# Performance work log

Measured on AMD Instinct MI355X. Metric: run time of the kernel, lower is better.

## Reference

```python
import jax, jax.numpy as jnp
import numpy as np


def setup_inputs() -> dict:
    key = jax.random.key(0)
    k1, k2, k3, k4 = jax.random.split(key, 4)
    B, S, IN, OUT = 4, 512, 4096, 11008
    x = jax.random.normal(k1, (B, S, IN), dtype=jnp.float32)
    # int8-valued weights stored as int32 (symmetric per-output-channel quant)
    w_int8 = jax.random.randint(k2, (OUT, IN), -128, 128, dtype=jnp.int32)
    # per-output-channel fp32 scales (positive, like absmax/127)
    scales = jax.random.uniform(k3, (OUT,), dtype=jnp.float32, minval=1e-4, maxval=0.05)
    bias = jax.random.normal(k4, (OUT,), dtype=jnp.float32)
    return {"x": x, "w_int8": w_int8, "scales": scales, "bias": bias}


def reference(x, w_int8, scales, bias):
    # On-the-fly dequant: w[o, i] = int8[o, i] * scale[o], then y = x @ w.T + b
    w = (w_int8.astype(jnp.float32) * scales[:, None]).astype(x.dtype)  # [OUT, IN]
    return jnp.einsum('bsi,oi->bso', x, w) + bias
```

## Files before the change

### kernel.cpp

```cpp
#include <hip/hip_runtime.h>
#include <hip/hip_bf16.h>
#include <stdint.h>


typedef __attribute__((ext_vector_type(8))) short short8;
typedef __attribute__((ext_vector_type(4))) float f32x4;
typedef __attribute__((ext_vector_type(4))) float float4v;
typedef __attribute__((ext_vector_type(4))) int int4v;

#define MM 2048
#define NN 11008
#define KK 4096
#define NT (KK / 64)
#define ROWB ((size_t)KK)

static __device__ __forceinline__ ushort f2bf_rne(float f) {
    uint32_t u = __builtin_bit_cast(uint32_t, f);
    u = (u + 0x7FFFu + ((u >> 16) & 1u)) >> 16;
    return (ushort)u;
}
static __device__ __forceinline__ ushort i2bf_exact(int v) {
    return (ushort)(__builtin_bit_cast(uint32_t, (float)v) >> 16);
}
static __device__ __forceinline__ void gload16(const void* g, void* lds) {
    __builtin_amdgcn_global_load_lds(
        (const __attribute__((address_space(1))) uint32_t*)g,
        (__attribute__((address_space(3))) uint32_t*)lds, 16, 0, 0);
}

#define BAR() do { asm volatile("" ::: "memory"); __builtin_amdgcn_s_barrier(); asm volatile("" ::: "memory"); } while (0)

__global__ __launch_bounds__(256)
void rowmax_x(const float* __restrict__ X, float* __restrict__ Sx, float* __restrict__ SxInv) {
    const int r = blockIdx.x;
    const float4v* xr = (const float4v*)(X + (size_t)r * KK);
    float m = 0.f;
    for (int i = threadIdx.x; i < KK / 4; i += 256) {
        float4v v = xr[i];
        m = fmaxf(m, fmaxf(fmaxf(fabsf(v[0]), fabsf(v[1])),
                           fmaxf(fabsf(v[2]), fabsf(v[3]))));
    }
#pragma unroll
    for (int off = 32; off; off >>= 1) m = fmaxf(m, __shfl_down(m, off));
    __shared__ float wmax[4];
    if ((threadIdx.x & 63) == 0) wmax[threadIdx.x >> 6] = m;
    __syncthreads();
    if (threadIdx.x == 0) {
        float a = fmaxf(fmaxf(wmax[0], wmax[1]), fmaxf(wmax[2], wmax[3]));
        Sx[r]    = a / 127.f;
        SxInv[r] = (a > 0.f) ? 127.f / a : 0.f;
    }
}

__global__ __launch_bounds__(256)
void quant_pack(const float* __restrict__ X, const int* __restrict__ W,
                const float* __restrict__ SxInv,
                char* __restrict__ Xq, char* __restrict__ Wq) {
    const int NX4 = MM * KK / 4;
    const int NW4 = NN * KK / 4;
    const int stride = gridDim.x * blockDim.x;
    for (int i = blockIdx.x * blockDim.x + threadIdx.x; i < NX4 + NW4; i += stride) {
        if (i < NX4) {
            float4v v = ((const float4v*)X)[i];
            const float inv = SxInv[i >> 10];
            uint32_t p = 0;
#pragma unroll
            for (int j = 0; j < 4; ++j) {
                int q = (int)rintf(v[j] * inv);
                p |= ((uint32_t)(q & 255)) << (8 * j);
            }
            ((uint32_t*)Xq)[i] = p;
        } else {
            int j = i - NX4;
            int4v w = ((const int4v*)W)[j];
            uint32_t p = ((uint32_t)(w[0] & 255)) | ((uint32_t)(w[1] & 255) << 8) |
                         ((uint32_t)(w[2] & 255) << 16) | ((uint32_t)(w[3] & 255) << 24);
            ((uint32_t*)Wq)[j] = p;
        }
    }
}

static __device__ __forceinline__ void stageA(const char* g, char* lds, int wid, size_t kb) {
    gload16(g + kb,                      lds        + wid * 1024);
    gload16(g + kb + (size_t)64 * ROWB,  lds + 4096 + wid * 1024);
}
static __device__ __forceinline__ void stageB(const char* g, char* lds, int wid, size_t kb) {
#pragma unroll
    for (int c = 0; c < 4; ++c)
        gload16(g + kb + (size_t)(c * 64) * ROWB, lds + c * 4096 + wid * 1024);
}

__global__ __launch_bounds__(256, 2)
void gemm_i8(const char* __restrict__ A, const char* __restrict__ B,
             const float* __restrict__ Sx, const float* __restrict__ S,
             const float* __restrict__ Bv, float* __restrict__ Y) {
    __shared__ char smem[73728];
    char* bA0 = smem;
    char* bA1 = smem + 8192;
    char* bA2 = smem + 16384;
    char* bB0 = smem + 24576;
    char* bB1 = smem + 40960;
    char* bB2 = smem + 57344;

    const int tid  = threadIdx.x;
    const int lane = tid & 63;
    const int wid  = tid >> 6;
    const int l15  = lane & 15;
    const int q    = lane >> 4;

    const int swz  = (blockIdx.x & 7) * 86 + (blockIdx.x >> 3);
    const int brow = (swz / 43) * 128;
    const int bcol = (swz % 43) * 256;

    const int srow4 = tid >> 2;
    const int sslot = (tid & 3) ^ ((srow4 >> 1) & 3);
    const char* gA = A + (size_t)(brow + srow4) * ROWB + sslot * 16;
    const char* gB = B + (size_t)(bcol + srow4) * ROWB + sslot * 16;

    const int kq  = (q ^ ((l15 >> 1) & 3)) * 16;
    const int rdA = l15 * 64;
    const int rdB = (wid * 64 + l15) * 64;

#define LDA(buf, m) (*(const int4v*)((buf) + rdA + (m) * 1024 + kq))
#define LDB(buf, n) (*(const int4v*)((buf) + rdB + (n) * 1024 + kq))

    int4v acc[8][4] = {};

    stageA(gA, bA0, wid, 0);
    stageB(gB, bB0, wid, 0);
    stageA(gA, bA1, wid, 64);
    stageB(gB, bB1, wid, 64);
    asm volatile("s_waitcnt vmcnt(6)" ::: "memory");
    BAR();

    char* cA = bA0; char* nA = bA1; char* pA = bA2;
    char* cB = bB0; char* nB = bB1; char* pB = bB2;

    for (int t = 0; t < NT; ++t) {
        const size_t kb2 = (size_t)((t + 2 < NT) ? t + 2 : NT - 1) * 64;

        int4v af[8], bf[4];
#pragma unroll
        for (int m = 0; m < 8; ++m) af[m] = LDA(cA, m);
#pragma unroll
        for (int n = 0; n < 4; ++n) bf[n] = LDB(cB, n);

        stageA(gA, pA, wid, kb2);
        stageB(gB, pB, wid, kb2);

        __builtin_amdgcn_s_setprio(1);
#pragma unroll
        for (int m = 0; m < 8; ++m)
#pragma unroll
            for (int n = 0; n < 4; ++n)
                acc[m][n] = __builtin_amdgcn_mfma_i32_16x16x64_i8(af[m], bf[n], acc[m][n], 0, 0, 0);
        __builtin_amdgcn_s_setprio(0);

        asm volatile("s_waitcnt vmcnt(6)" ::: "memory");
        BAR();

        char* tmp;
        tmp = cA; cA = nA; nA = pA; pA = tmp;
        tmp = cB; cB = nB; nB = pB; pB = tmp;
    }

#pragma unroll
    for (int n = 0; n < 4; ++n) {
        const int gc = bcol + wid * 64 + n * 16 + l15;
        const float sj = S[gc];
        const float bj = Bv[gc];
#pragma unroll
        for (int m = 0; m < 8; ++m) {
            const int grow = brow + m * 16 + q * 4;
            float* yp = Y + (size_t)grow * NN + gc;
#pragma unroll
            for (int r = 0; r < 4; ++r)
                yp[(size_t)r * NN] = (float)acc[m][n][r] * (Sx[grow + r] * sj) + bj;
        }
    }
#undef LDA
#undef LDB
}

#define BMF 128
#define BKF 32
#define LDW (BKF + 8)
__global__ __launch_bounds__(256, 2)
void int8lin_fused(const float* __restrict__ X, const int* __restrict__ W,
                   const float* __restrict__ S, const float* __restrict__ Bv,
                   float* __restrict__ Y) {
    __shared__ ushort As[BMF][LDW];
    __shared__ ushort Bs[BMF][LDW];
    const int tid = threadIdx.x, lane = tid & 63, wid = tid >> 6;
    const int wm = wid >> 1, wn = wid & 1, l15 = lane & 15, kh = (lane >> 4) * 8;
    const int bm = blockIdx.x & 15, bn = blockIdx.x >> 4;
    const int brow = bm * BMF, bcol = bn * BMF;
    const int srow = tid >> 1, scol = (tid & 1) * 16;
    const float* xg = X + (size_t)(brow + srow) * KK + scol;
    const int*   wg = W + (size_t)(bcol + srow) * KK + scol;
    f32x4 acc[4][4] = {};
    for (int kt = 0; kt < KK / BKF; ++kt) {
        float4v x0 = *(const float4v*)(xg + 0), x1 = *(const float4v*)(xg + 4);
        float4v x2 = *(const float4v*)(xg + 8), x3 = *(const float4v*)(xg + 12);
        int4v w0 = *(const int4v*)(wg + 0), w1 = *(const int4v*)(wg + 4);
        int4v w2 = *(const int4v*)(wg + 8), w3 = *(const int4v*)(wg + 12);
        xg += BKF; wg += BKF;
        short8 xa = { (short)f2bf_rne(x0[0]), (short)f2bf_rne(x0[1]), (short)f2bf_rne(x0[2]), (short)f2bf_rne(x0[3]),
                      (short)f2bf_rne(x1[0]), (short)f2bf_rne(x1[1]), (short)f2bf_rne(x1[2]), (short)f2bf_rne(x1[3]) };
        short8 xb = { (short)f2bf_rne(x2[0]), (short)f2bf_rne(x2[1]), (short)f2bf_rne(x2[2]), (short)f2bf_rne(x2[3]),
                      (short)f2bf_rne(x3[0]), (short)f2bf_rne(x3[1]), (short)f2bf_rne(x3[2]), (short)f2bf_rne(x3[3]) };
        short8 wa = { (short)i2bf_exact(w0[0]), (short)i2bf_exact(w0[1]), (short)i2bf_exact(w0[2]), (short)i2bf_exact(w0[3]),
                      (short)i2bf_exact(w1[0]), (short)i2bf_exact(w1[1]), (short)i2bf_exact(w1[2]), (short)i2bf_exact(w1[3]) };
        short8 wb = { (short)i2bf_exact(w2[0]), (short)i2bf_exact(w2[1]), (short)i2bf_exact(w2[2]), (short)i2bf_exact(w2[3]),
                      (short)i2bf_exact(w3[0]), (short)i2bf_exact(w3[1]), (short)i2bf_exact(w3[2]), (short)i2bf_exact(w3[3]) };
        __syncthreads();
        *(short8*)&As[srow][scol] = xa; *(short8*)&As[srow][scol + 8] = xb;
        *(short8*)&Bs[srow][scol] = wa; *(short8*)&Bs[srow][scol + 8] = wb;
        __syncthreads();
        short8 af2[4], bf4[4];
#pragma unroll
        for (int i = 0; i < 4; ++i) af2[i] = *(const short8*)&As[wm * 64 + i * 16 + l15][kh];
#pragma unroll
        for (int j = 0; j < 4; ++j) bf4[j] = *(const short8*)&Bs[wn * 64 + j * 16 + l15][kh];
#pragma unroll
        for (int i = 0; i < 4; ++i)
#pragma unroll
            for (int j = 0; j < 4; ++j)
                acc[i][j] = __builtin_amdgcn_mfma_f32_16x16x32_bf16(af2[i], bf4[j], acc[i][j], 0, 0, 0);
    }
#pragma unroll
    for (int j = 0; j < 4; ++j) {
        const int gc = bcol + wn * 64 + j * 16 + l15;
        const float sj = S[gc], bj = Bv[gc];
#pragma unroll
        for (int i = 0; i < 4; ++i) {
            const int grow = brow + wm * 64 + i * 16 + (lane >> 4) * 4;
            float* yp = Y + (size_t)grow * NN + gc;
#pragma unroll
            for (int r = 0; r < 4; ++r)
                yp[(size_t)r * NN] = acc[i][j][r] * sj + bj;
        }
    }
}

extern "C" void kernel_launch(void* const* d_in, const int* in_sizes, int n_in,
                              void* d_out, int out_size, void* d_ws, size_t ws_size,
                              hipStream_t stream) {
    const float* x = (const float*)d_in[0];
    const int*   w = (const int*)d_in[1];
    const float* s = (const float*)d_in[2];
    const float* b = (const float*)d_in[3];
    float* y = (float*)d_out;

    const size_t wq_b = (size_t)NN * KK;
    const size_t xq_b = (size_t)MM * KK;
    const size_t need = wq_b + xq_b + 2 * MM * sizeof(float) + 256;
    if (ws_size >= need) {
        char*  Wq    = (char*)d_ws;
        char*  Xq    = Wq + wq_b;
        float* Sx    = (float*)(Xq + xq_b);
        float* SxInv = Sx + MM;
        hipLaunchKernelGGL(rowmax_x,   dim3(MM),   dim3(256), 0, stream, x, Sx, SxInv);
        hipLaunchKernelGGL(quant_pack, dim3(4096), dim3(256), 0, stream, x, w, SxInv, Xq, Wq);
        hipLaunchKernelGGL(gemm_i8, dim3((MM / 128) * (NN / 256)), dim3(256), 0, stream,
                           Xq, Wq, Sx, s, b, y);
    } else {
        hipLaunchKernelGGL(int8lin_fused, dim3((MM / BMF) * (NN / BMF)), dim3(256), 0, stream,
                           x, w, s, b, y);
    }
}
```

Baseline: 178.7 us.

## Software-pipeline LDS fragment loads across K-iterations with double-buffered registers

```diff
diff --git a/kernel.cpp b/kernel.cpp
--- a/kernel.cpp
+++ b/kernel.cpp
@@ -95,12 +95,6 @@
              const float* __restrict__ Sx, const float* __restrict__ S,
              const float* __restrict__ Bv, float* __restrict__ Y) {
     __shared__ char smem[73728];
-    char* bA0 = smem;
-    char* bA1 = smem + 8192;
-    char* bA2 = smem + 16384;
-    char* bB0 = smem + 24576;
-    char* bB1 = smem + 40960;
-    char* bB2 = smem + 57344;
 
     const int tid  = threadIdx.x;
     const int lane = tid & 63;
@@ -125,44 +119,60 @@
 #define LDB(buf, n) (*(const int4v*)((buf) + rdB + (n) * 1024 + kq))
 
     int4v acc[8][4] = {};
-
-    stageA(gA, bA0, wid, 0);
-    stageB(gB, bB0, wid, 0);
-    stageA(gA, bA1, wid, 64);
-    stageB(gB, bB1, wid, 64);
+    int4v afA_a[4], afA_b[4], bf_a[4], bf_b[4], afB[4];
+
+    char* cA = smem;              char* cB = smem + 24576;
+    char* nA = smem + 8192;       char* nB = smem + 40960;
+    char* pA = smem + 16384;      char* pB = smem + 57344;
+
+    stageA(gA, cA, wid, 0);
+    stageB(gB, cB, wid, 0);
+    stageA(gA, nA, wid, 64);
+    stageB(gB, nB, wid, 64);
     asm volatile("s_waitcnt vmcnt(6)" ::: "memory");
     BAR();
-
-    char* cA = bA0; char* nA = bA1; char* pA = bA2;
-    char* cB = bB0; char* nB = bB1; char* pB = bB2;
-
-    for (int t = 0; t < NT; ++t) {
-        const size_t kb2 = (size_t)((t + 2 < NT) ? t + 2 : NT - 1) * 64;
-
-        int4v af[8], bf[4];
-#pragma unroll
-        for (int m = 0; m < 8; ++m) af[m] = LDA(cA, m);
-#pragma unroll
-        for (int n = 0; n < 4; ++n) bf[n] = LDB(cB, n);
-
-        stageA(gA, pA, wid, kb2);
-        stageB(gB, pB, wid, kb2);
-
-        __builtin_amdgcn_s_setprio(1);
-#pragma unroll
-        for (int m = 0; m < 8; ++m)
-#pragma unroll
-            for (int n = 0; n < 4; ++n)
-                acc[m][n] = __builtin_amdgcn_mfma_i32_16x16x64_i8(af[m], bf[n], acc[m][n], 0, 0, 0);
-        __builtin_amdgcn_s_setprio(0);
-
-        asm volatile("s_waitcnt vmcnt(6)" ::: "memory");
-        BAR();
-
-        char* tmp;
-        tmp = cA; cA = nA; nA = pA; pA = tmp;
-        tmp = cB; cB = nB; nB = pB; pB = tmp;
-    }
+#pragma unroll
+    for (int m = 0; m < 4; ++m) afA_a[m] = LDA(cA, m);
+#pragma unroll
+    for (int n = 0; n < 4; ++n) bf_a[n]  = LDB(cB, n);
+
+#define GEMM_ITER(AFAc, BFc, AFAn, BFn, T)                                        \
+    {                                                                             \
+        const int tt = (T);                                                       \
+        const size_t kb2 = (size_t)((tt + 2 < NT) ? tt + 2 : NT - 1) * 64;        \
+        _Pragma("unroll")                                                         \
+        for (int m = 0; m < 4; ++m) afB[m] = LDA(cA, m + 4);                      \
+        __builtin_amdgcn_s_setprio(1);                                            \
+        _Pragma("unroll")                                                         \
+        for (int m = 0; m < 4; ++m)                                               \
+            _Pragma("unroll")                                                     \
+            for (int n = 0; n < 4; ++n)                                           \
+                acc[m][n] = __builtin_amdgcn_mfma_i32_16x16x64_i8(AFAc[m], BFc[n], acc[m][n], 0, 0, 0); \
+        __builtin_amdgcn_s_setprio(0);                                            \
+        stageA(gA, pA, wid, kb2);                                                 \
+        stageB(gB, pB, wid, kb2);                                                 \
+        asm volatile("s_waitcnt vmcnt(6)" ::: "memory");                          \
+        BAR();                                                                    \
+        _Pragma("unroll")                                                         \
+        for (int m = 0; m < 4; ++m) AFAn[m] = LDA(nA, m);                         \
+        _Pragma("unroll")                                                         \
+        for (int n = 0; n < 4; ++n) BFn[n]  = LDB(nB, n);                         \
+        __builtin_amdgcn_s_setprio(1);                                            \
+        _Pragma("unroll")                                                         \
+        for (int m = 0; m < 4; ++m)                                               \
+            _Pragma("unroll")                                                     \
+            for (int n = 0; n < 4; ++n)                                           \
+                acc[m + 4][n] = __builtin_amdgcn_mfma_i32_16x16x64_i8(afB[m], BFc[n], acc[m + 4][n], 0, 0, 0); \
+        __builtin_amdgcn_s_setprio(0);                                            \
+        { char* t0 = cA; cA = nA; nA = pA; pA = t0;                               \
+          char* t1 = cB; cB = nB; nB = pB; pB = t1; }                             \
+    }
+
+    for (int t = 0; t < NT; t += 2) {
+        GEMM_ITER(afA_a, bf_a, afA_b, bf_b, t);
+        GEMM_ITER(afA_b, bf_b, afA_a, bf_a, t + 1);
+    }
+#undef GEMM_ITER
 
 #pragma unroll
     for (int n = 0; n < 4; ++n) {
```

After: 182.6 us. 2.2% more time.
